# Optimization experiments

Hardware: AMD Instinct MI355X
Metric: run time of the kernel (lower is better)

## Reference

```python
import jax, jax.numpy as jnp
import numpy as np

HIDDEN = 1024
SENT = 1024
NS = 8192
NK = 8192


def setup_inputs() -> dict:
    key = jax.random.key(0)
    ks = jax.random.split(key, 6)
    scale = 0.02
    return {
        "sentences_embedding": jax.random.normal(ks[0], (NS, SENT), dtype=jnp.float32),
        "knowledge_embedding": jax.random.normal(ks[1], (NK, 2 * HIDDEN), dtype=jnp.float32),
        "Ws": jax.random.normal(ks[2], (HIDDEN, SENT), dtype=jnp.float32) * scale,
        "bs": jnp.zeros((HIDDEN,), dtype=jnp.float32),
        "Wk": jax.random.normal(ks[3], (HIDDEN, 2 * HIDDEN), dtype=jnp.float32) * scale,
        "bk": jnp.zeros((HIDDEN,), dtype=jnp.float32),
    }


def reference(sentences_embedding, knowledge_embedding, Ws, bs, Wk, bk):
    # S: [Ns, hidden], K: [Nk, hidden] (torch Linear: x @ W.T + b)
    S = sentences_embedding @ Ws.T + bs
    K = knowledge_embedding @ Wk.T + bk
    V = knowledge_embedding  # [Nk, 2*hidden]
    scores = S @ K.T  # [Ns, Nk]
    # NOTE: softmax over dim=0 (across sentences), per the original module
    attns = jax.nn.softmax(scores, axis=0)
    fused_knowledge = attns @ V  # [Ns, 2*hidden]
    return (attns, fused_knowledge)
```

## Files before the change

### kernel.cpp

```cpp
#include <hip/hip_runtime.h>
#include <hip/hip_bf16.h>
#include <math.h>

typedef __bf16 bf16_t;
typedef __bf16 bf16x8 __attribute__((ext_vector_type(8)));
typedef __bf16 bf16x4v __attribute__((ext_vector_type(4)));
typedef float floatx4 __attribute__((ext_vector_type(4)));

#define BM 128
#define BN 128
#define BK 64
#define LDT 72

__device__ __forceinline__ void gload_lds16(const void* g, void* l) {
    __builtin_amdgcn_global_load_lds(
        (__attribute__((address_space(1))) void*)g,
        (__attribute__((address_space(3))) void*)l,
        16, 0, 0);
}

__device__ __forceinline__ void xcd_swizzle(int gx, int gy, int& bx, int& by) {
    const int nwg = gx * gy;
    const int bid = (int)blockIdx.y * gx + (int)blockIdx.x;
    const int cpx = nwg >> 3;
    const int s   = (bid & 7) * cpx + (bid >> 3);
    bx = s % gx;
    by = s / gx;
}

__device__ __forceinline__ void split8(const float* p, bf16x8& hi, bf16x8& lo) {
    const float4* q = (const float4*)p;
    float4 a = q[0], b = q[1];
    float v[8] = { a.x, a.y, a.z, a.w, b.x, b.y, b.z, b.w };
#pragma unroll
    for (int i = 0; i < 8; ++i) {
        bf16_t h = (bf16_t)v[i];
        hi[i] = h;
        lo[i] = (bf16_t)(v[i] - (float)h);
    }
}

template<bool OUT_SPLIT, bool HAS_BIAS>
__global__ __launch_bounds__(256, 2)
void gemm_nt_split(const float* __restrict__ A, const float* __restrict__ B,
                   const float* __restrict__ bias,
                   void* __restrict__ C0, bf16_t* __restrict__ Clo,
                   int M, int N, int K, int gx, int gy)
{
    __shared__ bf16_t Ah[BM * LDT];
    __shared__ bf16_t Al[BM * LDT];
    __shared__ bf16_t Bh[BN * LDT];
    __shared__ bf16_t Bl[BN * LDT];

    int bx, by;
    xcd_swizzle(gx, gy, bx, by);

    const int t    = threadIdx.x;
    const int m0   = bx * BM;
    const int n0   = by * BN;
    const int lane = t & 63;
    const int wm   = ((t >> 6) & 1) * 64;
    const int wn   = (t >> 7) * 64;
    const int lr   = lane & 15;
    const int lg   = lane >> 4;

    floatx4 acc[4][4] = {};

    for (int k0 = 0; k0 < K; k0 += BK) {
#pragma unroll
        for (int i = 0; i < 4; ++i) {
            int idx = t + i * 256;
            int row = idx >> 3;
            int col = (idx & 7) << 3;
            bf16x8 h, l;
            split8(&A[(size_t)(m0 + row) * K + k0 + col], h, l);
            *(bf16x8*)&Ah[row * LDT + col] = h;
            *(bf16x8*)&Al[row * LDT + col] = l;
            split8(&B[(size_t)(n0 + row) * K + k0 + col], h, l);
            *(bf16x8*)&Bh[row * LDT + col] = h;
            *(bf16x8*)&Bl[row * LDT + col] = l;
        }
        __syncthreads();
#pragma unroll
        for (int ks = 0; ks < BK; ks += 32) {
            bf16x8 ah[4], al[4], bh[4], bl[4];
#pragma unroll
            for (int mi = 0; mi < 4; ++mi) {
                ah[mi] = *(const bf16x8*)&Ah[(wm + mi * 16 + lr) * LDT + ks + lg * 8];
                al[mi] = *(const bf16x8*)&Al[(wm + mi * 16 + lr) * LDT + ks + lg * 8];
            }
#pragma unroll
            for (int ni = 0; ni < 4; ++ni) {
                bh[ni] = *(const bf16x8*)&Bh[(wn + ni * 16 + lr) * LDT + ks + lg * 8];
                bl[ni] = *(const bf16x8*)&Bl[(wn + ni * 16 + lr) * LDT + ks + lg * 8];
            }
#pragma unroll
            for (int mi = 0; mi < 4; ++mi)
#pragma unroll
                for (int ni = 0; ni < 4; ++ni) {
                    acc[mi][ni] = __builtin_amdgcn_mfma_f32_16x16x32_bf16(ah[mi], bh[ni], acc[mi][ni], 0, 0, 0);
                    acc[mi][ni] = __builtin_amdgcn_mfma_f32_16x16x32_bf16(ah[mi], bl[ni], acc[mi][ni], 0, 0, 0);
                    acc[mi][ni] = __builtin_amdgcn_mfma_f32_16x16x32_bf16(al[mi], bh[ni], acc[mi][ni], 0, 0, 0);
                }
        }
        __syncthreads();
    }

#pragma unroll
    for (int mi = 0; mi < 4; ++mi)
#pragma unroll
        for (int ni = 0; ni < 4; ++ni) {
            int col = n0 + wn + ni * 16 + lr;
            float bv = 0.0f;
            if constexpr (HAS_BIAS) bv = bias[col];
#pragma unroll
            for (int r = 0; r < 4; ++r) {
                int row = m0 + wm + mi * 16 + lg * 4 + r;
                float v = acc[mi][ni][r] + bv;
                if constexpr (OUT_SPLIT) {
                    bf16_t h = (bf16_t)v;
                    ((bf16_t*)C0)[(size_t)row * N + col] = h;
                    Clo[(size_t)row * N + col] = (bf16_t)(v - (float)h);
                } else {
                    ((float*)C0)[(size_t)row * N + col] = v;
                }
            }
        }
}

__global__ __launch_bounds__(256, 2)
void gemm_nt_pre_async(const bf16_t* __restrict__ Ahi, const bf16_t* __restrict__ Alo,
                       const bf16_t* __restrict__ Bhi, const bf16_t* __restrict__ Blo,
                       float* __restrict__ C, float* __restrict__ pm,
                       float* __restrict__ pz, int M, int N, int K, int gx, int gy)
{
    __shared__ bf16_t Ah[BM * BK];
    __shared__ bf16_t Al[BM * BK];
    __shared__ bf16_t Bh[BN * BK];
    __shared__ bf16_t Bl[BN * BK];
    __shared__ float red_m[2][128];
    __shared__ float red_z[2][128];

    int bx, by;
    xcd_swizzle(gx, gy, bx, by);

    const int t    = threadIdx.x;
    const int m0   = bx * BM;
    const int n0   = by * BN;
    const int lane = t & 63;
    const int wv   = t >> 6;
    const int widm = (t >> 6) & 1;
    const int wm   = widm * 64;
    const int wn   = (t >> 7) * 64;
    const int lr   = lane & 15;
    const int lg   = lane >> 4;
    const int lrow = lane >> 3;
    const int lcol = (((lane & 7) ^ lrow) * 8);
    const int swz  = (lr & 7) << 3;

    floatx4 acc[4][4] = {};

    for (int k0 = 0; k0 < K; k0 += BK) {
#pragma unroll
        for (int i = 0; i < 4; ++i) {
            const int seg = wv * 4 + i;
            const int row = seg * 8 + lrow;
            const size_t ga = (size_t)(m0 + row) * K + k0 + lcol;
            const size_t gb = (size_t)(n0 + row) * K + k0 + lcol;
            gload_lds16(&Ahi[ga], &Ah[seg * 512]);
            gload_lds16(&Alo[ga], &Al[seg * 512]);
            gload_lds16(&Bhi[gb], &Bh[seg * 512]);
            gload_lds16(&Blo[gb], &Bl[seg * 512]);
        }
        __syncthreads();
#pragma unroll
        for (int ks = 0; ks < BK; ks += 32) {
            const int cA = (ks + lg * 8) ^ swz;
            bf16x8 ah[4], al[4], bh[4], bl[4];
#pragma unroll
            for (int mi = 0; mi < 4; ++mi) {
                ah[mi] = *(const bf16x8*)&Ah[(wm + mi * 16 + lr) * BK + cA];
                al[mi] = *(const bf16x8*)&Al[(wm + mi * 16 + lr) * BK + cA];
            }
#pragma unroll
            for (int ni = 0; ni < 4; ++ni) {
                bh[ni] = *(const bf16x8*)&Bh[(wn + ni * 16 + lr) * BK + cA];
                bl[ni] = *(const bf16x8*)&Bl[(wn + ni * 16 + lr) * BK + cA];
            }
#pragma unroll
            for (int mi = 0; mi < 4; ++mi)
#pragma unroll
                for (int ni = 0; ni < 4; ++ni) {
                    acc[mi][ni] = __builtin_amdgcn_mfma_f32_16x16x32_bf16(ah[mi], bh[ni], acc[mi][ni], 0, 0, 0);
                    acc[mi][ni] = __builtin_amdgcn_mfma_f32_16x16x32_bf16(ah[mi], bl[ni], acc[mi][ni], 0, 0, 0);
                    acc[mi][ni] = __builtin_amdgcn_mfma_f32_16x16x32_bf16(al[mi], bh[ni], acc[mi][ni], 0, 0, 0);
                }
        }
        __syncthreads();
    }

#pragma unroll
    for (int mi = 0; mi < 4; ++mi)
#pragma unroll
        for (int ni = 0; ni < 4; ++ni) {
            int col = n0 + wn + ni * 16 + lr;
#pragma unroll
            for (int r = 0; r < 4; ++r) {
                int row = m0 + wm + mi * 16 + lg * 4 + r;
                C[(size_t)row * N + col] = acc[mi][ni][r];
            }
        }

#pragma unroll
    for (int ni = 0; ni < 4; ++ni) {
        float lm = -INFINITY;
#pragma unroll
        for (int mi = 0; mi < 4; ++mi)
#pragma unroll
            for (int r = 0; r < 4; ++r) lm = fmaxf(lm, acc[mi][ni][r]);
        float lz = 0.0f;
#pragma unroll
        for (int mi = 0; mi < 4; ++mi)
#pragma unroll
            for (int r = 0; r < 4; ++r) lz += __expf(acc[mi][ni][r] - lm);
#pragma unroll
        for (int off = 16; off <= 32; off <<= 1) {
            float om = __shfl_xor(lm, off);
            float oz = __shfl_xor(lz, off);
            float nm = fmaxf(lm, om);
            lz = lz * __expf(lm - nm) + oz * __expf(om - nm);
            lm = nm;
        }
        if (lg == 0) {
            red_m[widm][wn + ni * 16 + lr] = lm;
            red_z[widm][wn + ni * 16 + lr] = lz;
        }
    }
    __syncthreads();
    if (t < 128) {
        float a = red_m[0][t], b = red_m[1][t];
        float za = red_z[0][t], zb = red_z[1][t];
        float mb = fmaxf(a, b);
        float z  = za * __expf(a - mb) + zb * __expf(b - mb);
        pm[(size_t)bx * 8192 + n0 + t] = mb;
        pz[(size_t)bx * 8192 + n0 + t] = z;
    }
}

__global__ __launch_bounds__(256, 2)
void gemm_nt_bf16_async(const bf16_t* __restrict__ A, const bf16_t* __restrict__ B,
                        float* __restrict__ C, int M, int N, int K, int gx, int gy)
{
    __shared__ bf16_t As[BM * BK];
    __shared__ bf16_t Bs[BN * BK];

    int bx, by;
    xcd_swizzle(gx, gy, bx, by);

    const int t    = threadIdx.x;
    const int m0   = bx * BM;
    const int n0   = by * BN;
    const int lane = t & 63;
    const int wv   = t >> 6;
    const int wm   = ((t >> 6) & 1) * 64;
    const int wn   = (t >> 7) * 64;
    const int lr   = lane & 15;
    const int lg   = lane >> 4;
    const int lrow = lane >> 3;
    const int lcol = (((lane & 7) ^ lrow) * 8);
    const int swz  = (lr & 7) << 3;

    floatx4 acc[4][4] = {};

    for (int k0 = 0; k0 < K; k0 += BK) {
#pragma unroll
        for (int i = 0; i < 4; ++i) {
            const int seg = wv * 4 + i;
            const int row = seg * 8 + lrow;
            gload_lds16(&A[(size_t)(m0 + row) * K + k0 + lcol], &As[seg * 512]);
            gload_lds16(&B[(size_t)(n0 + row) * K + k0 + lcol], &Bs[seg * 512]);
        }
        __syncthreads();
#pragma unroll
        for (int ks = 0; ks < BK; ks += 32) {
            const int cA = (ks + lg * 8) ^ swz;
            bf16x8 a[4], b[4];
#pragma unroll
            for (int mi = 0; mi < 4; ++mi)
                a[mi] = *(const bf16x8*)&As[(wm + mi * 16 + lr) * BK + cA];
#pragma unroll
            for (int ni = 0; ni < 4; ++ni)
                b[ni] = *(const bf16x8*)&Bs[(wn + ni * 16 + lr) * BK + cA];
#pragma unroll
            for (int mi = 0; mi < 4; ++mi)
#pragma unroll
                for (int ni = 0; ni < 4; ++ni)
                    acc[mi][ni] = __builtin_amdgcn_mfma_f32_16x16x32_bf16(
                        a[mi], b[ni], acc[mi][ni], 0, 0, 0);
        }
        __syncthreads();
    }

#pragma unroll
    for (int mi = 0; mi < 4; ++mi)
#pragma unroll
        for (int ni = 0; ni < 4; ++ni) {
            int col = n0 + wn + ni * 16 + lr;
#pragma unroll
            for (int r = 0; r < 4; ++r) {
                int row = m0 + wm + mi * 16 + lg * 4 + r;
                C[(size_t)row * N + col] = acc[mi][ni][r];
            }
        }
}

__global__ __launch_bounds__(256)
void transpose_to_bf16(const float* __restrict__ src, bf16_t* __restrict__ dst,
                       int R, int Ccols)
{
    __shared__ float tile[64][65];
    const int r0 = blockIdx.x * 64;
    const int c0 = blockIdx.y * 64;
    const int tr = threadIdx.x >> 4;
    const int tc = (threadIdx.x & 15) * 4;
#pragma unroll
    for (int i = 0; i < 4; ++i) {
        int r = tr + i * 16;
        float4 v = *(const float4*)&src[(size_t)(r0 + r) * Ccols + c0 + tc];
        tile[r][tc + 0] = v.x; tile[r][tc + 1] = v.y;
        tile[r][tc + 2] = v.z; tile[r][tc + 3] = v.w;
    }
    __syncthreads();
#pragma unroll
    for (int i = 0; i < 4; ++i) {
        int c = tr + i * 16;
        bf16x4v o = { (bf16_t)tile[tc + 0][c], (bf16_t)tile[tc + 1][c],
                      (bf16_t)tile[tc + 2][c], (bf16_t)tile[tc + 3][c] };
        *(bf16x4v*)&dst[(size_t)(c0 + c) * R + r0 + tc] = o;
    }
}

__global__ __launch_bounds__(256)
void col_softmax_combine64(const float* __restrict__ pm, const float* __restrict__ pz,
                           float* __restrict__ mf, float* __restrict__ iz)
{
    int j = blockIdx.x * 256 + threadIdx.x;
    float m = -INFINITY;
#pragma unroll
    for (int c = 0; c < 64; ++c) m = fmaxf(m, pm[(size_t)c * 8192 + j]);
    float z = 0.0f;
#pragma unroll
    for (int c = 0; c < 64; ++c) z += pz[(size_t)c * 8192 + j] * __expf(pm[(size_t)c * 8192 + j] - m);
    mf[j] = m;
    iz[j] = 1.0f / z;
}

__global__ __launch_bounds__(256)
void normalize_attn_bf16(float* __restrict__ sc, const float* __restrict__ mf,
                         const float* __restrict__ iz, bf16_t* __restrict__ ab)
{
    size_t base = ((size_t)blockIdx.x * 256 + threadIdx.x) * 4;
    int j = (int)(base & 8191);
    float4 s  = *(float4*)&sc[base];
    float4 m4 = *(const float4*)&mf[j];
    float4 z4 = *(const float4*)&iz[j];
    s.x = __expf(s.x - m4.x) * z4.x;
    s.y = __expf(s.y - m4.y) * z4.y;
    s.z = __expf(s.z - m4.z) * z4.z;
    s.w = __expf(s.w - m4.w) * z4.w;
    *(float4*)&sc[base] = s;
    bf16x4v b = { (bf16_t)s.x, (bf16_t)s.y, (bf16_t)s.z, (bf16_t)s.w };
    *(bf16x4v*)&ab[base] = b;
}

extern "C" void kernel_launch(void* const* d_in, const int* in_sizes, int n_in,
                              void* d_out, int out_size, void* d_ws, size_t ws_size,
                              hipStream_t stream) {
    const float* sent  = (const float*)d_in[0];
    const float* knowl = (const float*)d_in[1];
    const float* Ws    = (const float*)d_in[2];
    const float* bs    = (const float*)d_in[3];
    const float* Wk    = (const float*)d_in[4];
    const float* bk    = (const float*)d_in[5];

    float* attns = (float*)d_out;
    float* fused = (float*)d_out + (size_t)8192 * 8192;

    const size_t MB = 1024 * 1024;
    char* ws = (char*)d_ws;
    dim3 blk(256);

    bf16_t* Shi = (bf16_t*)(ws + 0 * MB);
    bf16_t* Slo = (bf16_t*)(ws + 16 * MB);
    bf16_t* Khi = (bf16_t*)(ws + 32 * MB);
    bf16_t* Klo = (bf16_t*)(ws + 48 * MB);
    bf16_t* Ab  = (bf16_t*)(ws);
    bf16_t* Vt  = (bf16_t*)(ws + 128 * MB);
    float*  pm  = (float*)(ws + 160 * MB);
    float*  pz  = (float*)(ws + 162 * MB);
    float*  mf  = (float*)(ws + 164 * MB);
    float*  iz  = mf + 8192;

    gemm_nt_split<true, true><<<dim3(64, 8), blk, 0, stream>>>(
        sent, Ws, bs, Shi, Slo, 8192, 1024, 1024, 64, 8);
    gemm_nt_split<true, true><<<dim3(64, 8), blk, 0, stream>>>(
        knowl, Wk, bk, Khi, Klo, 8192, 1024, 2048, 64, 8);
    gemm_nt_pre_async<<<dim3(64, 64), blk, 0, stream>>>(
        Shi, Slo, Khi, Klo, attns, pm, pz, 8192, 8192, 1024, 64, 64);
    transpose_to_bf16<<<dim3(128, 32), blk, 0, stream>>>(knowl, Vt, 8192, 2048);
    col_softmax_combine64<<<dim3(32), blk, 0, stream>>>(pm, pz, mf, iz);
    normalize_attn_bf16<<<dim3(65536), blk, 0, stream>>>(attns, mf, iz, Ab);
    gemm_nt_bf16_async<<<dim3(64, 16), blk, 0, stream>>>(
        Ab, Vt, fused, 8192, 2048, 8192, 64, 16);
}
```

Measured before the change: 1.367 ms.

## Merge projections and V transpose into one launch; drop XCD swizzle

Folds the two projection GEMMs and the V transpose into a single kernel that picks its segment from the block index, so the three independent prep stages share one launch and can overlap on the GPU. It also removes the XCD-aware block-index swizzle from the large attention-score and output GEMMs and uses the raw block coordinates. The fused kernel reserves the projection kernel's larger shared-memory footprint and launch bounds for the transpose blocks as well, which may lower their occupancy. Dropping the swizzle may reduce L2 locality on the multi-XCD chip.

Measured after the change: 1.352 ms. No clear change (-1.1%).

```diff
diff --git a/kernel.cpp b/kernel.cpp
--- a/kernel.cpp
+++ b/kernel.cpp
@@ -19,15 +19,6 @@
         16, 0, 0);
 }
 
-__device__ __forceinline__ void xcd_swizzle(int gx, int gy, int& bx, int& by) {
-    const int nwg = gx * gy;
-    const int bid = (int)blockIdx.y * gx + (int)blockIdx.x;
-    const int cpx = nwg >> 3;
-    const int s   = (bid & 7) * cpx + (bid >> 3);
-    bx = s % gx;
-    by = s / gx;
-}
-
 __device__ __forceinline__ void split8(const float* p, bf16x8& hi, bf16x8& lo) {
     const float4* q = (const float4*)p;
     float4 a = q[0], b = q[1];
@@ -40,20 +31,16 @@
     }
 }
 
-template<bool OUT_SPLIT, bool HAS_BIAS>
-__global__ __launch_bounds__(256, 2)
-void gemm_nt_split(const float* __restrict__ A, const float* __restrict__ B,
-                   const float* __restrict__ bias,
-                   void* __restrict__ C0, bf16_t* __restrict__ Clo,
-                   int M, int N, int K, int gx, int gy)
-{
-    __shared__ bf16_t Ah[BM * LDT];
-    __shared__ bf16_t Al[BM * LDT];
-    __shared__ bf16_t Bh[BN * LDT];
-    __shared__ bf16_t Bl[BN * LDT];
-
-    int bx, by;
-    xcd_swizzle(gx, gy, bx, by);
+__device__ void proj_segment(char* smem,
+                             const float* __restrict__ A, const float* __restrict__ B,
+                             const float* __restrict__ bias,
+                             bf16_t* __restrict__ Chi, bf16_t* __restrict__ Clo,
+                             int M, int N, int K, int bx, int by)
+{
+    bf16_t* Ah = (bf16_t*)smem;
+    bf16_t* Al = Ah + BM * LDT;
+    bf16_t* Bh = Al + BM * LDT;
+    bf16_t* Bl = Bh + BN * LDT;
 
     const int t    = threadIdx.x;
     const int m0   = bx * BM;
@@ -111,28 +98,73 @@
 #pragma unroll
         for (int ni = 0; ni < 4; ++ni) {
             int col = n0 + wn + ni * 16 + lr;
-            float bv = 0.0f;
-            if constexpr (HAS_BIAS) bv = bias[col];
+            float bv = bias[col];
 #pragma unroll
             for (int r = 0; r < 4; ++r) {
                 int row = m0 + wm + mi * 16 + lg * 4 + r;
                 float v = acc[mi][ni][r] + bv;
-                if constexpr (OUT_SPLIT) {
-                    bf16_t h = (bf16_t)v;
-                    ((bf16_t*)C0)[(size_t)row * N + col] = h;
-                    Clo[(size_t)row * N + col] = (bf16_t)(v - (float)h);
-                } else {
-                    ((float*)C0)[(size_t)row * N + col] = v;
-                }
-            }
-        }
+                bf16_t h = (bf16_t)v;
+                Chi[(size_t)row * N + col] = h;
+                Clo[(size_t)row * N + col] = (bf16_t)(v - (float)h);
+            }
+        }
+}
+
+__device__ void transpose_segment(char* smem,
+                                  const float* __restrict__ src, bf16_t* __restrict__ dst,
+                                  int R, int Ccols, int tbx, int tby)
+{
+    float (*tile)[65] = (float (*)[65])smem;
+    const int r0 = tbx * 64;
+    const int c0 = tby * 64;
+    const int tr = threadIdx.x >> 4;
+    const int tc = (threadIdx.x & 15) * 4;
+#pragma unroll
+    for (int i = 0; i < 4; ++i) {
+        int r = tr + i * 16;
+        float4 v = *(const float4*)&src[(size_t)(r0 + r) * Ccols + c0 + tc];
+        tile[r][tc + 0] = v.x; tile[r][tc + 1] = v.y;
+        tile[r][tc + 2] = v.z; tile[r][tc + 3] = v.w;
+    }
+    __syncthreads();
+#pragma unroll
+    for (int i = 0; i < 4; ++i) {
+        int c = tr + i * 16;
+        bf16x4v o = { (bf16_t)tile[tc + 0][c], (bf16_t)tile[tc + 1][c],
+                      (bf16_t)tile[tc + 2][c], (bf16_t)tile[tc + 3][c] };
+        *(bf16x4v*)&dst[(size_t)(c0 + c) * R + r0 + tc] = o;
+    }
+}
+
+__global__ __launch_bounds__(256, 2)
+void prep_fused(const float* __restrict__ sent, const float* __restrict__ Ws,
+                const float* __restrict__ bs,
+                const float* __restrict__ knowl, const float* __restrict__ Wk,
+                const float* __restrict__ bk,
+                bf16_t* __restrict__ Shi, bf16_t* __restrict__ Slo,
+                bf16_t* __restrict__ Khi, bf16_t* __restrict__ Klo,
+                bf16_t* __restrict__ Vt)
+{
+    __shared__ char smem[4 * BM * LDT * sizeof(bf16_t)];
+    const int bid = blockIdx.x;
+    if (bid < 512) {
+        proj_segment(smem, sent, Ws, bs, Shi, Slo, 8192, 1024, 1024,
+                     bid & 63, bid >> 6);
+    } else if (bid < 1024) {
+        const int b = bid - 512;
+        proj_segment(smem, knowl, Wk, bk, Khi, Klo, 8192, 1024, 2048,
+                     b & 63, b >> 6);
+    } else {
+        const int b = bid - 1024;
+        transpose_segment(smem, knowl, Vt, 8192, 2048, b & 127, b >> 7);
+    }
 }
 
 __global__ __launch_bounds__(256, 2)
 void gemm_nt_pre_async(const bf16_t* __restrict__ Ahi, const bf16_t* __restrict__ Alo,
                        const bf16_t* __restrict__ Bhi, const bf16_t* __restrict__ Blo,
                        float* __restrict__ C, float* __restrict__ pm,
-                       float* __restrict__ pz, int M, int N, int K, int gx, int gy)
+                       float* __restrict__ pz, int M, int N, int K)
 {
     __shared__ bf16_t Ah[BM * BK];
     __shared__ bf16_t Al[BM * BK];
@@ -141,12 +173,9 @@
     __shared__ float red_m[2][128];
     __shared__ float red_z[2][128];
 
-    int bx, by;
-    xcd_swizzle(gx, gy, bx, by);
-
     const int t    = threadIdx.x;
-    const int m0   = bx * BM;
-    const int n0   = by * BN;
+    const int m0   = blockIdx.x * BM;
+    const int n0   = blockIdx.y * BN;
     const int lane = t & 63;
     const int wv   = t >> 6;
     const int widm = (t >> 6) & 1;
@@ -242,24 +271,21 @@
         float za = red_z[0][t], zb = red_z[1][t];
         float mb = fmaxf(a, b);
         float z  = za * __expf(a - mb) + zb * __expf(b - mb);
-        pm[(size_t)bx * 8192 + n0 + t] = mb;
-        pz[(size_t)bx * 8192 + n0 + t] = z;
+        pm[(size_t)blockIdx.x * 8192 + n0 + t] = mb;
+        pz[(size_t)blockIdx.x * 8192 + n0 + t] = z;
     }
 }
 
 __global__ __launch_bounds__(256, 2)
 void gemm_nt_bf16_async(const bf16_t* __restrict__ A, const bf16_t* __restrict__ B,
-                        float* __restrict__ C, int M, int N, int K, int gx, int gy)
+                        float* __restrict__ C, int M, int N, int K)
 {
     __shared__ bf16_t As[BM * BK];
     __shared__ bf16_t Bs[BN * BK];
 
-    int bx, by;
-    xcd_swizzle(gx, gy, bx, by);
-
     const int t    = threadIdx.x;
-    const int m0   = bx * BM;
-    const int n0   = by * BN;
+    const int m0   = blockIdx.x * BM;
+    const int n0   = blockIdx.y * BN;
     const int lane = t & 63;
     const int wv   = t >> 6;
     const int wm   = ((t >> 6) & 1) * 64;
@@ -312,32 +338,6 @@
                 C[(size_t)row * N + col] = acc[mi][ni][r];
             }
         }
-}
-
-__global__ __launch_bounds__(256)
-void transpose_to_bf16(const float* __restrict__ src, bf16_t* __restrict__ dst,
-                       int R, int Ccols)
-{
-    __shared__ float tile[64][65];
-    const int r0 = blockIdx.x * 64;
-    const int c0 = blockIdx.y * 64;
-    const int tr = threadIdx.x >> 4;
-    const int tc = (threadIdx.x & 15) * 4;
-#pragma unroll
-    for (int i = 0; i < 4; ++i) {
-        int r = tr + i * 16;
-        float4 v = *(const float4*)&src[(size_t)(r0 + r) * Ccols + c0 + tc];
-        tile[r][tc + 0] = v.x; tile[r][tc + 1] = v.y;
-        tile[r][tc + 2] = v.z; tile[r][tc + 3] = v.w;
-    }
-    __syncthreads();
-#pragma unroll
-    for (int i = 0; i < 4; ++i) {
-        int c = tr + i * 16;
-        bf16x4v o = { (bf16_t)tile[tc + 0][c], (bf16_t)tile[tc + 1][c],
-                      (bf16_t)tile[tc + 2][c], (bf16_t)tile[tc + 3][c] };
-        *(bf16x4v*)&dst[(size_t)(c0 + c) * R + r0 + tc] = o;
-    }
 }
 
 __global__ __launch_bounds__(256)
@@ -401,15 +401,12 @@
     float*  mf  = (float*)(ws + 164 * MB);
     float*  iz  = mf + 8192;
 
-    gemm_nt_split<true, true><<<dim3(64, 8), blk, 0, stream>>>(
-        sent, Ws, bs, Shi, Slo, 8192, 1024, 1024, 64, 8);
-    gemm_nt_split<true, true><<<dim3(64, 8), blk, 0, stream>>>(
-        knowl, Wk, bk, Khi, Klo, 8192, 1024, 2048, 64, 8);
+    prep_fused<<<dim3(5120), blk, 0, stream>>>(
+        sent, Ws, bs, knowl, Wk, bk, Shi, Slo, Khi, Klo, Vt);
     gemm_nt_pre_async<<<dim3(64, 64), blk, 0, stream>>>(
-        Shi, Slo, Khi, Klo, attns, pm, pz, 8192, 8192, 1024, 64, 64);
-    transpose_to_bf16<<<dim3(128, 32), blk, 0, stream>>>(knowl, Vt, 8192, 2048);
+        Shi, Slo, Khi, Klo, attns, pm, pz, 8192, 8192, 1024);
     col_softmax_combine64<<<dim3(32), blk, 0, stream>>>(pm, pz, mf, iz);
     normalize_attn_bf16<<<dim3(65536), blk, 0, stream>>>(attns, mf, iz, Ab);
     gemm_nt_bf16_async<<<dim3(64, 16), blk, 0, stream>>>(
-        Ab, Vt, fused, 8192, 2048, 8192, 64, 16);
-}
+        Ab, Vt, fused, 8192, 2048, 8192);
+}
```
